# Performance work log

Measured on AMD Instinct MI355X. Metric: run time of the kernel, lower is better.

## Reference

```python
import jax, jax.numpy as jnp
import numpy as np

RADIUS = 1.0
NSAMPLE = 32


def setup_inputs() -> dict:
    key = jax.random.key(0)
    k1, k2, k3, k4, k5 = jax.random.split(key, 5)
    B, Nb, M, K, C = 2, 2048, 64, 216, 32
    N = B * Nb
    # points in a 20m cube
    xyz = jax.random.uniform(k1, (N, 3), dtype=jnp.float32) * 20.0
    xyz_batch_cnt = jnp.array([Nb, Nb], dtype=jnp.int32)
    # rois: [x,y,z,dx,dy,dz,ry]
    ctr = jax.random.uniform(k2, (B, M, 3), dtype=jnp.float32) * 20.0
    dims = 1.0 + jax.random.uniform(k3, (B, M, 3), dtype=jnp.float32) * 2.0
    ry = jax.random.uniform(k4, (B, M, 1), dtype=jnp.float32) * 6.28
    rois = jnp.concatenate([ctr, dims, ry], axis=-1)
    # 6x6x6 grid points jittered around each roi center
    off = (jax.random.uniform(k5, (B, M, K, 3), dtype=jnp.float32) - 0.5) * 3.0
    new_xyz = ctr[:, :, None, :] + off
    features = jax.random.normal(jax.random.fold_in(key, 7), (N, C), dtype=jnp.float32)
    return {"xyz": xyz, "xyz_batch_cnt": xyz_batch_cnt, "new_xyz": new_xyz,
            "rois": rois, "features": features}


def _query_and_group(xyz, new_xyz, rois, features, B, Nb):
    """Ball query -> ragged compaction (padded to L=N*nsample) -> gather."""
    M, K = new_xyz.shape[1], new_xyz.shape[2]
    MK = M * K
    N = B * Nb
    L = N * NSAMPLE
    xyz_b = xyz.reshape(B, Nb, 3)
    grid = new_xyz.reshape(B, MK, 3)
    # squared distances point -> grid center, (B, Nb, MK)
    d2 = jnp.sum((xyz_b[:, :, None, :] - grid[:, None, :, :]) ** 2, axis=-1)
    # roi bounding sphere: center rois[:,:,:3], radius ||dims||_2 (the `ball` tensor)
    ctr = rois[:, :, :3]
    r2 = jnp.sum(rois[:, :, 3:6] ** 2, axis=-1)          # (B, M)
    d2b = jnp.sum((xyz_b[:, :, None, :] - ctr[:, None, :, :]) ** 2, axis=-1)  # (B,Nb,M)
    in_ball = (d2b <= r2[:, None, :])[:, :, :, None]      # (B,Nb,M,1)
    mask = (d2 <= RADIUS * RADIUS) & jnp.broadcast_to(in_ball, (B, Nb, M, K)).reshape(B, Nb, MK)
    # first-NSAMPLE-in-order selection per point (matches kernel iteration order)
    rank = jnp.cumsum(mask.astype(jnp.int32), axis=2) - 1
    cols = jnp.where(mask & (rank < NSAMPLE), rank, NSAMPLE)  # NSAMPLE = OOB -> dropped
    rows = jnp.broadcast_to(
        jnp.arange(B, dtype=jnp.int32)[:, None, None] * Nb
        + jnp.arange(Nb, dtype=jnp.int32)[None, :, None], (B, Nb, MK))
    flat_idx = jnp.broadcast_to(
        jnp.arange(B, dtype=jnp.int32)[:, None, None] * MK
        + jnp.arange(MK, dtype=jnp.int32)[None, None, :], (B, Nb, MK))
    ball_idx = jnp.full((N, NSAMPLE), -1, dtype=jnp.int32)
    ball_idx = ball_idx.at[rows.reshape(-1), cols.reshape(-1)].set(
        flat_idx.reshape(-1), mode="drop")
    # BallIndice: cumsum compaction of valid (point_idx, grid_idx) pairs, row-major
    valid = (ball_idx > -1).reshape(-1)                  # (L,)
    pos = jnp.cumsum(valid.astype(jnp.int32)) - 1
    pos_w = jnp.where(valid, pos, L)                     # invalid -> OOB -> dropped
    row_ids = jnp.broadcast_to(
        jnp.arange(N, dtype=jnp.int32)[:, None], (N, NSAMPLE)).reshape(-1)
    set_indices = jnp.zeros((L,), jnp.int32).at[pos_w].set(row_ids, mode="drop")
    set_new_indices = jnp.zeros((L,), jnp.int32).at[pos_w].set(
        ball_idx.reshape(-1), mode="drop")
    nind = jnp.sum(valid.astype(jnp.int32))
    vm = (jnp.arange(L) < nind)[:, None].astype(features.dtype)  # padding mask
    # GatherFeature (padded slots zeroed, matching new_zeros semantics)
    group_xyz = xyz[set_indices] * vm
    group_new_xyz = new_xyz.reshape(-1, 3)[set_new_indices] * vm
    group_feat = features[set_indices] * vm
    group_features = jnp.concatenate([group_xyz - group_new_xyz, group_feat], axis=1)
    return group_features, set_new_indices


def reference(xyz, xyz_batch_cnt, new_xyz, rois, features):
    B = xyz_batch_cnt.shape[0]
    Nb = xyz.shape[0] // B
    return _query_and_group(xyz, new_xyz, rois, features, B, Nb)
```

## Files before the change

kernel.cpp:

```cpp
#include <hip/hip_runtime.h>


#pragma clang fp contract(off)

typedef unsigned long long u64;

#define MAXN 4096

__global__ __launch_bounds__(256) void count_kernel(
    const float* __restrict__ xyz, const float* __restrict__ new_xyz,
    const float* __restrict__ rois, int* __restrict__ counts,
    int* __restrict__ blockSums, int* __restrict__ ballidx,
    int N, int Nb, int M, int K, int nsample)
{
    __shared__ int plist[4][64];
    __shared__ int scnt[4];
    const int wave = threadIdx.x >> 6;
    const int lane = threadIdx.x & 63;
    const int r = blockIdx.x * 4 + wave;
    const u64 laneLt = (1ull << lane) - 1ull;

    int cntc = 0;
    if (r < N) {
        const int b  = r / Nb;
        const float px = xyz[3 * r + 0];
        const float py = xyz[3 * r + 1];
        const float pz = xyz[3 * r + 2];

        bool pass = false;
        if (lane < M) {
            const float* rp = rois + (size_t)(b * M + lane) * 7;
            const float dx = rp[3], dy = rp[4], dz = rp[5];
            const float r2 = (dx * dx + dy * dy) + dz * dz;
            const float ex = px - rp[0], ey = py - rp[1], ez = pz - rp[2];
            pass = ((ex * ex + ey * ey) + ez * ez) <= r2;
        }
        const u64 roiMask = __ballot(pass);
        if (roiMask) {
            if (pass) plist[wave][__popcll(roiMask & laneLt)] = lane;

            const int P = __popcll(roiMask);
            const int total = P * K;
            const float* nb_ = new_xyz + (size_t)(b * M * K) * 3;
            int* bi = ballidx + (size_t)r * nsample;

            int cnt = 0;
            for (int base = 0; base < total && cnt < nsample; base += 256) {
                bool match[4];
                int jj[4];
                #pragma unroll
                for (int u = 0; u < 4; u++) {
                    const int p = base + u * 64 + lane;
                    match[u] = false; jj[u] = 0;
                    if (p < total) {
                        const int ri = p / K;
                        const int k  = p - ri * K;
                        const int j  = plist[wave][ri] * K + k;
                        jj[u] = j;
                        const float* gp = nb_ + (size_t)j * 3;
                        const float ax = px - gp[0], ay = py - gp[1], az = pz - gp[2];
                        match[u] = ((ax * ax + ay * ay) + az * az) <= 1.0f;
                    }
                }
                #pragma unroll
                for (int u = 0; u < 4; u++) {
                    const u64 mm = __ballot(match[u]);
                    const int slot = cnt + __popcll(mm & laneLt);
                    if (match[u] && slot < nsample) bi[slot] = jj[u];
                    cnt += __popcll(mm);
                }
            }
            cntc = cnt > nsample ? nsample : cnt;
        }
        if (lane == 0) counts[r] = cntc;
    }
    if (lane == 0) scnt[wave] = cntc;
    __syncthreads();
    if (threadIdx.x == 0)
        blockSums[blockIdx.x] = scnt[0] + scnt[1] + scnt[2] + scnt[3];
}

__global__ __launch_bounds__(256) void emit_kernel(
    const float* __restrict__ xyz, const float* __restrict__ new_xyz,
    const float* __restrict__ features,
    const int* __restrict__ counts, const int* __restrict__ blockSums,
    const int* __restrict__ ballidx,
    float* __restrict__ out_feat, float* __restrict__ out_idx,
    int N, int Nb, int M, int K, int C, int nsample, int numBlocks)
{
    __shared__ int sred[8];
    const int t = threadIdx.x;
    const int lane = t & 63;
    const int wid = t >> 6;

    int pre = 0, tot = 0;
    {
        const int b0 = t * 4;
        #pragma unroll
        for (int i = 0; i < 4; i++) {
            const int bb = b0 + i;
            if (bb < numBlocks) {
                const int v = blockSums[bb];
                tot += v;
                if (bb < (int)blockIdx.x) pre += v;
            }
        }
        #pragma unroll
        for (int d = 1; d < 64; d <<= 1) {
            pre += __shfl_xor(pre, d, 64);
            tot += __shfl_xor(tot, d, 64);
        }
        if (lane == 0) { sred[wid] = pre; sred[4 + wid] = tot; }
    }
    __syncthreads();
    const int blockPre = sred[0] + sred[1] + sred[2] + sred[3];
    const int nind     = sred[4] + sred[5] + sred[6] + sred[7];

    const int W = 3 + C;
    const size_t L = (size_t)N * nsample;
    const int r0 = blockIdx.x * 4;
    const int r  = r0 + wid;

    if (r < N) {
        const int cnt = counts[r];
        if (cnt > 0) {
            int rowpre = 0;
            if (lane < wid && (r0 + lane) < N) rowpre = counts[r0 + lane];
            #pragma unroll
            for (int d = 1; d < 64; d <<= 1) rowpre += __shfl_xor(rowpre, d, 64);

            const int b  = r / Nb;
            const int MK = M * K;
            const int obase = blockPre + rowpre;
            const int* bi = ballidx + (size_t)r * nsample;
            const float px = xyz[3 * r + 0];
            const float py = xyz[3 * r + 1];
            const float pz = xyz[3 * r + 2];
            const float* fr = features + (size_t)r * C;
            const float* nb_ = new_xyz + (size_t)b * MK * 3;

            float* dst = out_feat + (size_t)obase * W;
            const int totE = cnt * W;
            for (int idx = lane; idx < totE; idx += 64) {
                const int s = idx / W;
                const int c = idx - s * W;
                const int j = bi[s];
                float v;
                if (c == 0)      v = px - nb_[(size_t)j * 3 + 0];
                else if (c == 1) v = py - nb_[(size_t)j * 3 + 1];
                else if (c == 2) v = pz - nb_[(size_t)j * 3 + 2];
                else             v = fr[c - 3];
                dst[idx] = v;
            }
            for (int s = lane; s < cnt; s += 64)
                out_idx[obase + s] = (float)(b * MK + bi[s]);
        }
    }

    const int gtid = blockIdx.x * 256 + t;
    const int gthreads = gridDim.x * 256;
    {
        const size_t sA = (size_t)nind * W;
        const size_t eA = L * (size_t)W;
        if (sA < eA) {
            const size_t s4 = (sA + 3) & ~(size_t)3;
            const size_t headEnd = s4 < eA ? s4 : eA;
            if ((size_t)gtid < headEnd - sA) out_feat[sA + gtid] = 0.0f;
            if (s4 < eA) {
                const size_t nvec = (eA - s4) >> 2;
                float4* p4 = (float4*)(out_feat + s4);
                const float4 z = make_float4(0.0f, 0.0f, 0.0f, 0.0f);
                for (size_t i = gtid; i < nvec; i += gthreads) p4[i] = z;
                const size_t rem = (eA - s4) & 3;
                if ((size_t)gtid < rem) out_feat[eA - rem + gtid] = 0.0f;
            }
        }
    }
    for (size_t i = (size_t)nind + gtid; i < L; i += gthreads)
        out_idx[i] = 0.0f;
}

extern "C" void kernel_launch(void* const* d_in, const int* in_sizes, int n_in,
                              void* d_out, int out_size, void* d_ws, size_t ws_size,
                              hipStream_t stream) {
    if (n_in < 5) return;

    int bc = 0;
    for (int i = 1; i < n_in; i++) if (in_sizes[i] < in_sizes[bc]) bc = i;
    const int B = in_sizes[bc];
    if (B < 1) return;

    int xi = -1, nwi = -1, ri = -1, fi = -1;
    int N = 0, M = 0, K = 0, C = 0, nsample = 0;

    for (int rr = 0; rr < n_in && xi < 0; rr++) {
        if (rr == bc) continue;
        if (in_sizes[rr] % (7 * B)) continue;
        const int M_ = in_sizes[rr] / (7 * B);
        if (M_ < 1 || M_ > 64) continue;
        for (int xx = 0; xx < n_in && xi < 0; xx++) {
            if (xx == bc || xx == rr) continue;
            if (in_sizes[xx] % 3) continue;
            const int N_ = in_sizes[xx] / 3;
            if (N_ < B || N_ % B || N_ > MAXN) continue;
            for (int nn = 0; nn < n_in && xi < 0; nn++) {
                if (nn == bc || nn == rr || nn == xx) continue;
                if (in_sizes[nn] % (3 * B * M_)) continue;
                const int K_ = in_sizes[nn] / (3 * B * M_);
                if (K_ < 1) continue;
                for (int ff = 0; ff < n_in && xi < 0; ff++) {
                    if (ff == bc || ff == rr || ff == xx || ff == nn) continue;
                    if (in_sizes[ff] % N_) continue;
                    const int C_ = in_sizes[ff] / N_;
                    if (C_ < 1) continue;
                    if (out_size % (4 + C_)) continue;
                    const long long L_ = (long long)out_size / (4 + C_);
                    if (L_ % N_) continue;
                    const int ns = (int)(L_ / N_);
                    if (ns < 1 || ns > 1024) continue;
                    xi = xx; nwi = nn; ri = rr; fi = ff;
                    N = N_; M = M_; K = K_; C = C_; nsample = ns;
                }
            }
        }
    }
    if (xi < 0) return;

    const float* xyz      = (const float*)d_in[xi];
    const float* new_xyz  = (const float*)d_in[nwi];
    const float* rois     = (const float*)d_in[ri];
    const float* features = (const float*)d_in[fi];
    const int Nb = N / B;

    const size_t L      = (size_t)N * nsample;
    const size_t chunk0 = L * (size_t)(3 + C);

    float* out_feat = (float*)d_out;
    float* out_idx  = out_feat + chunk0;

    const int blocks = (N + 3) / 4;

    const size_t wsNeed = ((size_t)N + (size_t)blocks + (size_t)N * nsample) * sizeof(int);
    if (ws_size < wsNeed) return;
    int* counts    = (int*)d_ws;
    int* blockSums = counts + N;
    int* ballidx   = blockSums + blocks;

    count_kernel<<<blocks, 256, 0, stream>>>(
        xyz, new_xyz, rois, counts, blockSums, ballidx,
        N, Nb, M, K, nsample);
    emit_kernel<<<blocks, 256, 0, stream>>>(
        xyz, new_xyz, features, counts, blockSums, ballidx,
        out_feat, out_idx, N, Nb, M, K, C, nsample, blocks);
}
```

Measured before the change: 88.11 us.

## Fuse count and emit kernels with cross-block spin-wait prefix sum

Merges the ball-query count kernel and the emit kernel into one launch. Each block publishes its per-block count to a descriptor array that a memset initialises to -1, and every block spins until all descriptors are filled before computing its prefix. Ball indices stay in LDS when nsample fits, and blocks shrink to 128 threads, with each wave handling two rows. This removes a kernel launch and the ballidx global round-trip, but adds a memset and a grid-wide spin that requires all 1024 blocks to be co-resident, otherwise it deadlocks.

New measurement: 104.9 us. 1.19x slower.

```diff
diff --git a/kernel.cpp b/kernel.cpp
--- a/kernel.cpp
+++ b/kernel.cpp
@@ -7,158 +7,177 @@
 
 #define MAXN 4096
 
-__global__ __launch_bounds__(256) void count_kernel(
+__global__ __launch_bounds__(128, 4) void fused_kernel(
     const float* __restrict__ xyz, const float* __restrict__ new_xyz,
-    const float* __restrict__ rois, int* __restrict__ counts,
-    int* __restrict__ blockSums, int* __restrict__ ballidx,
-    int N, int Nb, int M, int K, int nsample)
-{
-    __shared__ int plist[4][64];
-    __shared__ int scnt[4];
-    const int wave = threadIdx.x >> 6;
-    const int lane = threadIdx.x & 63;
-    const int r = blockIdx.x * 4 + wave;
-    const u64 laneLt = (1ull << lane) - 1ull;
-
-    int cntc = 0;
-    if (r < N) {
-        const int b  = r / Nb;
-        const float px = xyz[3 * r + 0];
-        const float py = xyz[3 * r + 1];
-        const float pz = xyz[3 * r + 2];
-
-        bool pass = false;
-        if (lane < M) {
-            const float* rp = rois + (size_t)(b * M + lane) * 7;
-            const float dx = rp[3], dy = rp[4], dz = rp[5];
-            const float r2 = (dx * dx + dy * dy) + dz * dz;
-            const float ex = px - rp[0], ey = py - rp[1], ez = pz - rp[2];
-            pass = ((ex * ex + ey * ey) + ez * ez) <= r2;
-        }
-        const u64 roiMask = __ballot(pass);
-        if (roiMask) {
-            if (pass) plist[wave][__popcll(roiMask & laneLt)] = lane;
-
-            const int P = __popcll(roiMask);
-            const int total = P * K;
-            const float* nb_ = new_xyz + (size_t)(b * M * K) * 3;
-            int* bi = ballidx + (size_t)r * nsample;
-
-            int cnt = 0;
-            for (int base = 0; base < total && cnt < nsample; base += 256) {
-                bool match[4];
-                int jj[4];
-                #pragma unroll
-                for (int u = 0; u < 4; u++) {
-                    const int p = base + u * 64 + lane;
-                    match[u] = false; jj[u] = 0;
-                    if (p < total) {
-                        const int ri = p / K;
-                        const int k  = p - ri * K;
-                        const int j  = plist[wave][ri] * K + k;
-                        jj[u] = j;
-                        const float* gp = nb_ + (size_t)j * 3;
-                        const float ax = px - gp[0], ay = py - gp[1], az = pz - gp[2];
-                        match[u] = ((ax * ax + ay * ay) + az * az) <= 1.0f;
-                    }
-                }
-                #pragma unroll
-                for (int u = 0; u < 4; u++) {
-                    const u64 mm = __ballot(match[u]);
-                    const int slot = cnt + __popcll(mm & laneLt);
-                    if (match[u] && slot < nsample) bi[slot] = jj[u];
-                    cnt += __popcll(mm);
-                }
-            }
-            cntc = cnt > nsample ? nsample : cnt;
-        }
-        if (lane == 0) counts[r] = cntc;
-    }
-    if (lane == 0) scnt[wave] = cntc;
-    __syncthreads();
-    if (threadIdx.x == 0)
-        blockSums[blockIdx.x] = scnt[0] + scnt[1] + scnt[2] + scnt[3];
-}
-
-__global__ __launch_bounds__(256) void emit_kernel(
-    const float* __restrict__ xyz, const float* __restrict__ new_xyz,
-    const float* __restrict__ features,
-    const int* __restrict__ counts, const int* __restrict__ blockSums,
-    const int* __restrict__ ballidx,
+    const float* __restrict__ rois, const float* __restrict__ features,
+    int* __restrict__ desc, int* __restrict__ ballidx,
     float* __restrict__ out_feat, float* __restrict__ out_idx,
     int N, int Nb, int M, int K, int C, int nsample, int numBlocks)
 {
-    __shared__ int sred[8];
-    const int t = threadIdx.x;
+    __shared__ int plist[2][64];
+    __shared__ int bis[4][64];
+    __shared__ int cnts[4];
+    __shared__ int sred[4];
+
+    const int t    = threadIdx.x;
+    const int wid  = t >> 6;
     const int lane = t & 63;
-    const int wid = t >> 6;
+    const int bid  = blockIdx.x;
+    const u64 laneLt = (1ull << lane) - 1ull;
+    const bool useLds = (nsample <= 64);
+
+    float rpx[2], rpy[2], rpz[2];
+    int   rcnt[2];
+
+    #pragma unroll
+    for (int q = 0; q < 2; q++) {
+        const int wrow = wid * 2 + q;
+        const int r = bid * 4 + wrow;
+        int cntc = 0;
+        rpx[q] = 0.0f; rpy[q] = 0.0f; rpz[q] = 0.0f;
+        if (r < N) {
+            const int b  = r / Nb;
+            const float px = xyz[3 * r + 0];
+            const float py = xyz[3 * r + 1];
+            const float pz = xyz[3 * r + 2];
+            rpx[q] = px; rpy[q] = py; rpz[q] = pz;
+
+            bool pass = false;
+            if (lane < M) {
+                const float* rp = rois + (size_t)(b * M + lane) * 7;
+                const float dx = rp[3], dy = rp[4], dz = rp[5];
+                const float r2 = (dx * dx + dy * dy) + dz * dz;
+                const float ex = px - rp[0], ey = py - rp[1], ez = pz - rp[2];
+                pass = ((ex * ex + ey * ey) + ez * ez) <= r2;
+            }
+            const u64 roiMask = __ballot(pass);
+            if (roiMask) {
+                if (pass) plist[wid][__popcll(roiMask & laneLt)] = lane;
+
+                const int P = __popcll(roiMask);
+                const int total = P * K;
+                const float* nb_ = new_xyz + (size_t)(b * M * K) * 3;
+                int* big = ballidx + (size_t)r * nsample;
+
+                int cnt = 0;
+                for (int base = 0; base < total && cnt < nsample; base += 256) {
+                    bool match[4];
+                    int jj[4];
+                    #pragma unroll
+                    for (int u = 0; u < 4; u++) {
+                        const int p = base + u * 64 + lane;
+                        match[u] = false; jj[u] = 0;
+                        if (p < total) {
+                            const int ri = p / K;
+                            const int k  = p - ri * K;
+                            const int j  = plist[wid][ri] * K + k;
+                            jj[u] = j;
+                            const float* gp = nb_ + (size_t)j * 3;
+                            const float ax = px - gp[0], ay = py - gp[1], az = pz - gp[2];
+                            match[u] = ((ax * ax + ay * ay) + az * az) <= 1.0f;
+                        }
+                    }
+                    #pragma unroll
+                    for (int u = 0; u < 4; u++) {
+                        const u64 mm = __ballot(match[u]);
+                        const int slot = cnt + __popcll(mm & laneLt);
+                        if (match[u] && slot < nsample) {
+                            if (useLds) bis[wrow][slot] = jj[u];
+                            else        big[slot] = jj[u];
+                        }
+                        cnt += __popcll(mm);
+                    }
+                }
+                cntc = cnt > nsample ? nsample : cnt;
+            }
+        }
+        rcnt[q] = cntc;
+        if (lane == 0) cnts[wrow] = cntc;
+    }
+    __syncthreads();
+
+    if (t == 0) {
+        const int agg = cnts[0] + cnts[1] + cnts[2] + cnts[3];
+        __hip_atomic_store(&desc[bid], agg, __ATOMIC_RELAXED, __HIP_MEMORY_SCOPE_AGENT);
+    }
 
     int pre = 0, tot = 0;
     {
-        const int b0 = t * 4;
+        unsigned pending = 0;
         #pragma unroll
-        for (int i = 0; i < 4; i++) {
-            const int bb = b0 + i;
-            if (bb < numBlocks) {
-                const int v = blockSums[bb];
-                tot += v;
-                if (bb < (int)blockIdx.x) pre += v;
-            }
+        for (int k = 0; k < 8; k++) {
+            const int idx = t + k * 128;
+            if (idx < numBlocks) pending |= (1u << k);
+        }
+        while (pending) {
+            #pragma unroll
+            for (int k = 0; k < 8; k++) {
+                if (pending & (1u << k)) {
+                    const int idx = t + k * 128;
+                    const int v = __hip_atomic_load(&desc[idx], __ATOMIC_RELAXED,
+                                                    __HIP_MEMORY_SCOPE_AGENT);
+                    if (v != -1) {
+                        pending &= ~(1u << k);
+                        tot += v;
+                        if (idx < bid) pre += v;
+                    }
+                }
+            }
+            if (pending) __builtin_amdgcn_s_sleep(8);
         }
         #pragma unroll
         for (int d = 1; d < 64; d <<= 1) {
             pre += __shfl_xor(pre, d, 64);
             tot += __shfl_xor(tot, d, 64);
         }
-        if (lane == 0) { sred[wid] = pre; sred[4 + wid] = tot; }
+        if (lane == 0) { sred[wid] = pre; sred[2 + wid] = tot; }
     }
     __syncthreads();
-    const int blockPre = sred[0] + sred[1] + sred[2] + sred[3];
-    const int nind     = sred[4] + sred[5] + sred[6] + sred[7];
-
-    const int W = 3 + C;
+    const int blockPre = sred[0] + sred[1];
+    const int nind     = sred[2] + sred[3];
+
+    const int W  = 3 + C;
     const size_t L = (size_t)N * nsample;
-    const int r0 = blockIdx.x * 4;
-    const int r  = r0 + wid;
-
-    if (r < N) {
-        const int cnt = counts[r];
-        if (cnt > 0) {
-            int rowpre = 0;
-            if (lane < wid && (r0 + lane) < N) rowpre = counts[r0 + lane];
-            #pragma unroll
-            for (int d = 1; d < 64; d <<= 1) rowpre += __shfl_xor(rowpre, d, 64);
-
-            const int b  = r / Nb;
-            const int MK = M * K;
-            const int obase = blockPre + rowpre;
-            const int* bi = ballidx + (size_t)r * nsample;
-            const float px = xyz[3 * r + 0];
-            const float py = xyz[3 * r + 1];
-            const float pz = xyz[3 * r + 2];
-            const float* fr = features + (size_t)r * C;
-            const float* nb_ = new_xyz + (size_t)b * MK * 3;
-
-            float* dst = out_feat + (size_t)obase * W;
-            const int totE = cnt * W;
-            for (int idx = lane; idx < totE; idx += 64) {
-                const int s = idx / W;
-                const int c = idx - s * W;
-                const int j = bi[s];
-                float v;
-                if (c == 0)      v = px - nb_[(size_t)j * 3 + 0];
-                else if (c == 1) v = py - nb_[(size_t)j * 3 + 1];
-                else if (c == 2) v = pz - nb_[(size_t)j * 3 + 2];
-                else             v = fr[c - 3];
-                dst[idx] = v;
-            }
-            for (int s = lane; s < cnt; s += 64)
-                out_idx[obase + s] = (float)(b * MK + bi[s]);
-        }
-    }
-
-    const int gtid = blockIdx.x * 256 + t;
-    const int gthreads = gridDim.x * 256;
+    const int MK = M * K;
+
+    #pragma unroll
+    for (int q = 0; q < 2; q++) {
+        const int wrow = wid * 2 + q;
+        const int r = bid * 4 + wrow;
+        if (r >= N) continue;
+        const int cnt = rcnt[q];
+        if (cnt <= 0) continue;
+
+        int rowpre = 0;
+        for (int i = 0; i < wrow; i++) rowpre += cnts[i];
+
+        const int b = r / Nb;
+        const int obase = blockPre + rowpre;
+        const int* big = ballidx + (size_t)r * nsample;
+        const float* fr  = features + (size_t)r * C;
+        const float* nb_ = new_xyz + (size_t)b * MK * 3;
+
+        float* dst = out_feat + (size_t)obase * W;
+        const int totE = cnt * W;
+        for (int idx = lane; idx < totE; idx += 64) {
+            const int s = idx / W;
+            const int c = idx - s * W;
+            const int j = useLds ? bis[wrow][s] : big[s];
+            float v;
+            if (c == 0)      v = rpx[q] - nb_[(size_t)j * 3 + 0];
+            else if (c == 1) v = rpy[q] - nb_[(size_t)j * 3 + 1];
+            else if (c == 2) v = rpz[q] - nb_[(size_t)j * 3 + 2];
+            else             v = fr[c - 3];
+            dst[idx] = v;
+        }
+        for (int s = lane; s < cnt; s += 64) {
+            const int j = useLds ? bis[wrow][s] : big[s];
+            out_idx[obase + s] = (float)(b * MK + j);
+        }
+    }
+
+    const int gtid = bid * 128 + t;
+    const size_t gthreads = (size_t)numBlocks * 128;
     {
         const size_t sA = (size_t)nind * W;
         const size_t eA = L * (size_t)W;
@@ -240,16 +259,14 @@
 
     const int blocks = (N + 3) / 4;
 
-    const size_t wsNeed = ((size_t)N + (size_t)blocks + (size_t)N * nsample) * sizeof(int);
+    const size_t wsNeed = ((size_t)blocks + (size_t)N * nsample) * sizeof(int);
     if (ws_size < wsNeed) return;
-    int* counts    = (int*)d_ws;
-    int* blockSums = counts + N;
-    int* ballidx   = blockSums + blocks;
-
-    count_kernel<<<blocks, 256, 0, stream>>>(
-        xyz, new_xyz, rois, counts, blockSums, ballidx,
-        N, Nb, M, K, nsample);
-    emit_kernel<<<blocks, 256, 0, stream>>>(
-        xyz, new_xyz, features, counts, blockSums, ballidx,
+    int* desc    = (int*)d_ws;
+    int* ballidx = desc + blocks;
+
+    hipMemsetAsync(desc, 0xFF, (size_t)blocks * sizeof(int), stream);
+
+    fused_kernel<<<blocks, 128, 0, stream>>>(
+        xyz, new_xyz, rois, features, desc, ballidx,
         out_feat, out_idx, N, Nb, M, K, C, nsample, blocks);
 }
```
